# Kernel tuning notes

Hardware: AMD Instinct MI355X
Metric: run time of the kernel (lower is better)

The kernel has to match this reference:

```python
import jax, jax.numpy as jnp
import numpy as np

B, T, D, K = 32, 2048, 1024, 31


def setup_inputs() -> dict:
    key = jax.random.key(0)
    ks = jax.random.split(key, 8)
    query = jax.random.normal(ks[0], (B, D), dtype=jnp.float32)
    memory = jax.random.normal(ks[1], (B, T, D), dtype=jnp.float32)
    prev_attn = jax.nn.softmax(jax.random.normal(ks[2], (B, T)), axis=-1).astype(jnp.float32)
    cum_attn = jax.random.uniform(ks[3], (B, T), dtype=jnp.float32)
    mask = jax.random.bernoulli(ks[4], 0.2, (B, T))
    mask = mask.at[:, 0].set(False)  # keep at least one valid position per row
    scale = 0.02
    Wq = jax.random.normal(ks[5], (D, D), dtype=jnp.float32) * scale    # torch Linear weight [out,in]
    Wm = jax.random.normal(ks[6], (D, D), dtype=jnp.float32) * scale
    k2 = jax.random.split(ks[7], 2)
    Wloc = jax.random.normal(k2[0], (D, 2, K), dtype=jnp.float32) * scale  # Conv1d weight [out_ch,in_ch,k]
    v = jax.random.normal(k2[1], (D,), dtype=jnp.float32) * scale          # Linear(d_model,1) weight squeezed
    return {"query": query, "memory": memory, "prev_attn": prev_attn,
            "cum_attn": cum_attn, "mask": mask,
            "Wq": Wq, "Wm": Wm, "Wloc": Wloc, "v": v}


def reference(query, memory, prev_attn, cum_attn, mask, Wq, Wm, Wloc, v):
    pad = Wloc.shape[-1] // 2
    # location features: [B,2,T] conv -> [B,D,T] -> [B,T,D]
    loc_in = jnp.stack([prev_attn, cum_attn], axis=1)
    loc = jax.lax.conv_general_dilated(
        loc_in, Wloc, window_strides=(1,), padding=[(pad, pad)],
        dimension_numbers=("NCW", "OIW", "NCW"))
    loc = jnp.transpose(loc, (0, 2, 1))                 # [B,T,D]
    q = (query @ Wq.T)[:, None, :]                      # [B,1,D]
    m = jnp.einsum("btd,ed->bte", memory, Wm)           # [B,T,D]
    e = jnp.einsum("btd,d->bt", jnp.tanh(q + m + loc), v)  # [B,T]
    e = jnp.where(mask, -jnp.inf, e)
    a = jax.nn.softmax(e, axis=1)                       # [B,T]
    ctx = jnp.einsum("bt,btd->bd", a, memory)           # [B,D]
    return ctx, a
```

## Files before the change

kernel.cpp:

```cpp
#include <hip/hip_runtime.h>
#include <math.h>

#define BATCH 32
#define T 2048
#define D 1024
#define KW 31
#define CPAD 15
#define KEXT 62
#define KEXTP 64
#define KTOT 1088
#define BM 128
#define BN 128
#define BK 32
#define NSTEP (KTOT / BK)

typedef __bf16 bf16_8 __attribute__((ext_vector_type(8)));
typedef __bf16 bf16_4 __attribute__((ext_vector_type(4)));
typedef float  f32x4  __attribute__((ext_vector_type(4)));

__device__ __forceinline__ float tanh_fast(float x) {
    return 1.f - 2.f * __builtin_amdgcn_rcpf(__expf(2.f * x) + 1.f);
}

__device__ __forceinline__ void glds16(const void* gsrc, void* ldst) {
    __builtin_amdgcn_global_load_lds(
        (const __attribute__((address_space(1))) unsigned int*)gsrc,
        (__attribute__((address_space(3))) unsigned int*)ldst, 16, 0, 0);
}

__global__ __launch_bounds__(256) void k_prep_b(const float* __restrict__ Wm,
                                                const float* __restrict__ Wloc,
                                                __bf16* __restrict__ Bext) {
    const int idx = blockIdx.x * 256 + threadIdx.x;
    const int d = idx / (KTOT / 4);
    const int kk = (idx % (KTOT / 4)) * 4;
    bf16_4 o;
    #pragma unroll
    for (int u = 0; u < 4; ++u) {
        const int k = kk + u;
        float val = 0.f;
        if (k < D) val = Wm[(size_t)d * D + k];
        else {
            const int j = k - D;
            if (j < KEXT) {
                const int c = (j >= KW) ? 1 : 0;
                const int kp = j - c * KW;
                val = Wloc[((size_t)d * 2 + c) * KW + kp];
            }
        }
        o[u] = (__bf16)val;
    }
    *(bf16_4*)(Bext + (size_t)d * KTOT + kk) = o;
}

__global__ __launch_bounds__(256) void k_prep_aloc(const float* __restrict__ prev,
                                                   const float* __restrict__ cum,
                                                   __bf16* __restrict__ Aloc) {
    const int idx = blockIdx.x * 256 + threadIdx.x;
    const int row = idx >> 4;
    const int j0 = (idx & 15) * 4;
    const int b = row >> 11;
    const int t = row & (T - 1);
    bf16_4 o;
    #pragma unroll
    for (int u = 0; u < 4; ++u) {
        const int j = j0 + u;
        float val = 0.f;
        if (j < KEXT) {
            const int c = (j >= KW) ? 1 : 0;
            const int kp = j - c * KW;
            const int ts = t + kp - CPAD;
            if (ts >= 0 && ts < T)
                val = (c ? cum : prev)[(size_t)b * T + ts];
        }
        o[u] = (__bf16)val;
    }
    *(bf16_4*)(Aloc + (size_t)row * KEXTP + j0) = o;
}

__global__ __launch_bounds__(256) void k_q(const float* __restrict__ query,
                                           const float* __restrict__ Wq,
                                           float* __restrict__ qout) {
    int b = blockIdx.y;
    int w = threadIdx.x >> 6;
    int lane = threadIdx.x & 63;
    int d = blockIdx.x * 4 + w;
    const float* qrow = query + (size_t)b * D;
    const float* wrow = Wq + (size_t)d * D;
    float s = 0.f;
    #pragma unroll
    for (int i = 0; i < D / 64; ++i) s += qrow[lane + i * 64] * wrow[lane + i * 64];
    #pragma unroll
    for (int off = 32; off > 0; off >>= 1) s += __shfl_down(s, off, 64);
    if (lane == 0) qout[(size_t)b * D + d] = s;
}

__global__ __launch_bounds__(256, 3) void k_gemm_e(
    const float* __restrict__ memory, const __bf16* __restrict__ Aloc,
    const __bf16* __restrict__ Bext, const float* __restrict__ qv,
    const float* __restrict__ vvec, float* __restrict__ e_part) {
    __shared__ bf16_8 As[3][512];
    __shared__ bf16_8 Bs[3][512];

    const int t0 = blockIdx.x * BM;
    const int d0 = blockIdx.y * BN;
    const int b  = blockIdx.z;
    const int tid  = threadIdx.x;
    const int lane = tid & 63;
    const int w    = tid >> 6;
    const int wr   = w >> 1, wc = w & 1;
    const int q    = lane >> 4, m = lane & 15;

    f32x4 acc[4][4] = {};

    const int g0 = w, g1 = w + 4;
    const size_t arow0 = (size_t)b * T + t0 + g0 * 16 + m;
    const size_t arow1 = (size_t)b * T + t0 + g1 * 16 + m;
    const float*  aptr0 = memory + arow0 * D + q * 8;
    const float*  aptr1 = memory + arow1 * D + q * 8;
    const __bf16* lptr0 = Aloc + arow0 * KEXTP + q * 8;
    const __bf16* lptr1 = Aloc + arow1 * KEXTP + q * 8;
    const __bf16* bptr0 = Bext + (size_t)(d0 + g0 * 16 + m) * KTOT + q * 8;
    const __bf16* bptr1 = Bext + (size_t)(d0 + g1 * 16 + m) * KTOT + q * 8;

    f32x4 pa[2][2];

    glds16(bptr0,      &Bs[0][g0 * 64]);
    glds16(bptr1,      &Bs[0][g1 * 64]);
    glds16(bptr0 + BK, &Bs[1][g0 * 64]);
    glds16(bptr1 + BK, &Bs[1][g1 * 64]);
    pa[0][0] = *(const f32x4*)(aptr0);
    pa[0][1] = *(const f32x4*)(aptr0 + 4);
    pa[1][0] = *(const f32x4*)(aptr1);
    pa[1][1] = *(const f32x4*)(aptr1 + 4);
    {
        bf16_8 c0, c1;
        #pragma unroll
        for (int i = 0; i < 4; ++i) {
            c0[i] = (__bf16)pa[0][0][i]; c0[i + 4] = (__bf16)pa[0][1][i];
            c1[i] = (__bf16)pa[1][0][i]; c1[i + 4] = (__bf16)pa[1][1][i];
        }
        As[0][g0 * 64 + lane] = c0;
        As[0][g1 * 64 + lane] = c1;
    }

    for (int k = 0; k < NSTEP; ++k) {
        const int p = k % 3;
        if (k > 0 && k * BK < D) {
            bf16_8 c0, c1;
            #pragma unroll
            for (int i = 0; i < 4; ++i) {
                c0[i] = (__bf16)pa[0][0][i]; c0[i + 4] = (__bf16)pa[0][1][i];
                c1[i] = (__bf16)pa[1][0][i]; c1[i + 4] = (__bf16)pa[1][1][i];
            }
            As[p][g0 * 64 + lane] = c0;
            As[p][g1 * 64 + lane] = c1;
        }
        __syncthreads();
        const int ka = k + 1;
        if (ka < NSTEP) {
            const int ka0 = ka * BK;
            if (ka0 < D) {
                pa[0][0] = *(const f32x4*)(aptr0 + ka0);
                pa[0][1] = *(const f32x4*)(aptr0 + ka0 + 4);
                pa[1][0] = *(const f32x4*)(aptr1 + ka0);
                pa[1][1] = *(const f32x4*)(aptr1 + ka0 + 4);
            } else {
                glds16(lptr0 + (ka0 - D), &As[ka % 3][g0 * 64]);
                glds16(lptr1 + (ka0 - D), &As[ka % 3][g1 * 64]);
            }
        }
        const int kb = k + 2;
        if (kb < NSTEP) {
            glds16(bptr0 + kb * BK, &Bs[kb % 3][g0 * 64]);
            glds16(bptr1 + kb * BK, &Bs[kb % 3][g1 * 64]);
        }
        bf16_8 af[4], bfr[4];
        #pragma unroll
        for (int i = 0; i < 4; ++i) af[i]  = As[p][(wr * 4 + i) * 64 + lane];
        #pragma unroll
        for (int j = 0; j < 4; ++j) bfr[j] = Bs[p][(wc * 4 + j) * 64 + lane];
        #pragma unroll
        for (int i = 0; i < 4; ++i)
            #pragma unroll
            for (int j = 0; j < 4; ++j)
                acc[i][j] = __builtin_amdgcn_mfma_f32_16x16x32_bf16(af[i], bfr[j], acc[i][j], 0, 0, 0);
    }

    float qreg[4], vreg[4];
    #pragma unroll
    for (int j = 0; j < 4; ++j) {
        const int d = d0 + wc * 64 + j * 16 + m;
        qreg[j] = qv[(size_t)b * D + d];
        vreg[j] = vvec[d];
    }
    const int dch = blockIdx.y * 2 + wc;
    #pragma unroll
    for (int i = 0; i < 4; ++i) {
        #pragma unroll
        for (int r = 0; r < 4; ++r) {
            float s = 0.f;
            #pragma unroll
            for (int j = 0; j < 4; ++j)
                s += tanh_fast(acc[i][j][r] + qreg[j]) * vreg[j];
            #pragma unroll
            for (int off = 8; off > 0; off >>= 1)
                s += __shfl_down(s, off, 16);
            if (m == 0) {
                const int t = t0 + wr * 64 + i * 16 + q * 4 + r;
                e_part[((size_t)b * T + t) * 16 + dch] = s;
            }
        }
    }
}

__global__ __launch_bounds__(256) void k_softmax(const float* __restrict__ e_part,
                                                 const int* __restrict__ mask,
                                                 float* __restrict__ aout) {
    const int b = blockIdx.x;
    const int tid = threadIdx.x;
    __shared__ float red[256];
    float ev[8];
    float lmax = -INFINITY;
    #pragma unroll
    for (int i = 0; i < 8; ++i) {
        const int t = tid + i * 256;
        const float* p = e_part + ((size_t)b * T + t) * 16;
        float s = 0.f;
        #pragma unroll
        for (int c = 0; c < 16; ++c) s += p[c];
        if (mask[(size_t)b * T + t] != 0) s = -INFINITY;
        ev[i] = s;
        lmax = fmaxf(lmax, s);
    }
    red[tid] = lmax; __syncthreads();
    for (int off = 128; off > 0; off >>= 1) {
        if (tid < off) red[tid] = fmaxf(red[tid], red[tid + off]);
        __syncthreads();
    }
    const float mx = red[0]; __syncthreads();
    float lsum = 0.f;
    #pragma unroll
    for (int i = 0; i < 8; ++i) {
        const float x = expf(ev[i] - mx);
        ev[i] = x;
        lsum += x;
    }
    red[tid] = lsum; __syncthreads();
    for (int off = 128; off > 0; off >>= 1) {
        if (tid < off) red[tid] += red[tid + off];
        __syncthreads();
    }
    const float inv = 1.f / red[0];
    #pragma unroll
    for (int i = 0; i < 8; ++i)
        aout[(size_t)b * T + tid + i * 256] = ev[i] * inv;
}

__global__ __launch_bounds__(256) void k_ctx_part(const float* __restrict__ memory,
                                                  const float* __restrict__ a,
                                                  float* __restrict__ ctx_part) {
    const int b = blockIdx.x;
    const int tc = blockIdx.y;
    const int d4 = threadIdx.x * 4;
    f32x4 acc = {0.f, 0.f, 0.f, 0.f};
    const float* mb = memory + ((size_t)b * T + (size_t)tc * 64) * D;
    const float* ab = a + (size_t)b * T + (size_t)tc * 64;
    #pragma unroll 4
    for (int t = 0; t < 64; ++t) {
        const float wgt = ab[t];
        const f32x4 m4 = *(const f32x4*)(mb + (size_t)t * D + d4);
        acc += wgt * m4;
    }
    *(f32x4*)(ctx_part + ((size_t)(b * 32 + tc)) * D + d4) = acc;
}

__global__ __launch_bounds__(256) void k_ctx_red(const float* __restrict__ ctx_part,
                                                 float* __restrict__ ctx) {
    const int idx = blockIdx.x * 256 + threadIdx.x;
    const int b = idx >> 10, d = idx & 1023;
    float s = 0.f;
    #pragma unroll
    for (int tc = 0; tc < 32; ++tc) s += ctx_part[((size_t)(b * 32 + tc)) * D + d];
    ctx[idx] = s;
}

extern "C" void kernel_launch(void* const* d_in, const int* in_sizes, int n_in,
                              void* d_out, int out_size, void* d_ws, size_t ws_size,
                              hipStream_t stream) {
    const float* query  = (const float*)d_in[0];
    const float* memory = (const float*)d_in[1];
    const float* prev   = (const float*)d_in[2];
    const float* cum    = (const float*)d_in[3];
    const int*   mask   = (const int*)d_in[4];
    const float* Wq     = (const float*)d_in[5];
    const float* Wm     = (const float*)d_in[6];
    const float* Wloc   = (const float*)d_in[7];
    const float* v      = (const float*)d_in[8];

    float* out = (float*)d_out;
    float* ctx = out;
    float* a   = out + BATCH * D;

    char* ws = (char*)d_ws;
    float*  qv       = (float*)(ws + 0);
    float*  e_part   = (float*)(ws + 131072);
    float*  ctx_part = (float*)(ws + 4325376);
    __bf16* Bext     = (__bf16*)(ws + 8519680);
    __bf16* Aloc     = (__bf16*)(ws + 10747904);

    k_prep_b<<<KTOT * D / (256 * 4), 256, 0, stream>>>(Wm, Wloc, Bext);
    k_prep_aloc<<<BATCH * T * 16 / 256, 256, 0, stream>>>(prev, cum, Aloc);
    k_q<<<dim3(D / 4, BATCH), 256, 0, stream>>>(query, Wq, qv);
    k_gemm_e<<<dim3(T / BM, D / BN, BATCH), 256, 0, stream>>>(memory, Aloc, Bext,
                                                              qv, v, e_part);
    k_softmax<<<BATCH, 256, 0, stream>>>(e_part, mask, a);
    k_ctx_part<<<dim3(BATCH, 32), 256, 0, stream>>>(memory, a, ctx_part);
    k_ctx_red<<<(BATCH * D) / 256, 256, 0, stream>>>(ctx_part, ctx);
}
```

Measured before the change: 759.7 us.

## Drop LDS staging in GEMM, load fragments directly from global, reorder grid

The energy GEMM no longer stages tiles in LDS with a triple-buffered async pipeline and barriers. Each wave now loads its A (fp32 memory, converted to bf16) and B fragments straight from global memory into registers, and the location-feature K tail becomes a separate loop. The grid is reordered so the D tiles of the same T rows run adjacently, which should improve L2 reuse of memory rows, and occupancy is raised to 4 blocks per CU. Without LDS sharing, each memory element is fetched by both column waves and B is fetched per row wave, which doubles global/L2 traffic. The softmax kernel also moves to 1024 threads with vectorised partial-sum loads.

Measured after the change: 1.073 ms. 41.2% more time.

```diff
diff --git a/kernel.cpp b/kernel.cpp
--- a/kernel.cpp
+++ b/kernel.cpp
@@ -12,7 +12,6 @@
 #define BM 128
 #define BN 128
 #define BK 32
-#define NSTEP (KTOT / BK)
 
 typedef __bf16 bf16_8 __attribute__((ext_vector_type(8)));
 typedef __bf16 bf16_4 __attribute__((ext_vector_type(4)));
@@ -20,12 +19,6 @@
 
 __device__ __forceinline__ float tanh_fast(float x) {
     return 1.f - 2.f * __builtin_amdgcn_rcpf(__expf(2.f * x) + 1.f);
-}
-
-__device__ __forceinline__ void glds16(const void* gsrc, void* ldst) {
-    __builtin_amdgcn_global_load_lds(
-        (const __attribute__((address_space(1))) unsigned int*)gsrc,
-        (__attribute__((address_space(3))) unsigned int*)ldst, 16, 0, 0);
 }
 
 __global__ __launch_bounds__(256) void k_prep_b(const float* __restrict__ Wm,
@@ -95,15 +88,12 @@
     if (lane == 0) qout[(size_t)b * D + d] = s;
 }
 
-__global__ __launch_bounds__(256, 3) void k_gemm_e(
+__global__ __launch_bounds__(256, 4) void k_gemm_e(
     const float* __restrict__ memory, const __bf16* __restrict__ Aloc,
     const __bf16* __restrict__ Bext, const float* __restrict__ qv,
     const float* __restrict__ vvec, float* __restrict__ e_part) {
-    __shared__ bf16_8 As[3][512];
-    __shared__ bf16_8 Bs[3][512];
-
-    const int t0 = blockIdx.x * BM;
-    const int d0 = blockIdx.y * BN;
+    const int d0 = blockIdx.x * BN;
+    const int t0 = blockIdx.y * BM;
     const int b  = blockIdx.z;
     const int tid  = threadIdx.x;
     const int lane = tid & 63;
@@ -113,73 +103,47 @@
 
     f32x4 acc[4][4] = {};
 
-    const int g0 = w, g1 = w + 4;
-    const size_t arow0 = (size_t)b * T + t0 + g0 * 16 + m;
-    const size_t arow1 = (size_t)b * T + t0 + g1 * 16 + m;
-    const float*  aptr0 = memory + arow0 * D + q * 8;
-    const float*  aptr1 = memory + arow1 * D + q * 8;
-    const __bf16* lptr0 = Aloc + arow0 * KEXTP + q * 8;
-    const __bf16* lptr1 = Aloc + arow1 * KEXTP + q * 8;
-    const __bf16* bptr0 = Bext + (size_t)(d0 + g0 * 16 + m) * KTOT + q * 8;
-    const __bf16* bptr1 = Bext + (size_t)(d0 + g1 * 16 + m) * KTOT + q * 8;
-
-    f32x4 pa[2][2];
-
-    glds16(bptr0,      &Bs[0][g0 * 64]);
-    glds16(bptr1,      &Bs[0][g1 * 64]);
-    glds16(bptr0 + BK, &Bs[1][g0 * 64]);
-    glds16(bptr1 + BK, &Bs[1][g1 * 64]);
-    pa[0][0] = *(const f32x4*)(aptr0);
-    pa[0][1] = *(const f32x4*)(aptr0 + 4);
-    pa[1][0] = *(const f32x4*)(aptr1);
-    pa[1][1] = *(const f32x4*)(aptr1 + 4);
-    {
-        bf16_8 c0, c1;
+    const float*  mb = memory + (size_t)b * T * D;
+    int aoff[4], boff[4];
+    #pragma unroll
+    for (int i = 0; i < 4; ++i)
+        aoff[i] = (t0 + wr * 64 + i * 16 + m) * D + q * 8;
+    #pragma unroll
+    for (int j = 0; j < 4; ++j)
+        boff[j] = (d0 + wc * 64 + j * 16 + m) * KTOT + q * 8;
+
+    #pragma unroll 2
+    for (int k0 = 0; k0 < D; k0 += BK) {
+        bf16_8 af[4], bfr[4];
         #pragma unroll
         for (int i = 0; i < 4; ++i) {
-            c0[i] = (__bf16)pa[0][0][i]; c0[i + 4] = (__bf16)pa[0][1][i];
-            c1[i] = (__bf16)pa[1][0][i]; c1[i + 4] = (__bf16)pa[1][1][i];
-        }
-        As[0][g0 * 64 + lane] = c0;
-        As[0][g1 * 64 + lane] = c1;
-    }
-
-    for (int k = 0; k < NSTEP; ++k) {
-        const int p = k % 3;
-        if (k > 0 && k * BK < D) {
-            bf16_8 c0, c1;
-            #pragma unroll
-            for (int i = 0; i < 4; ++i) {
-                c0[i] = (__bf16)pa[0][0][i]; c0[i + 4] = (__bf16)pa[0][1][i];
-                c1[i] = (__bf16)pa[1][0][i]; c1[i + 4] = (__bf16)pa[1][1][i];
+            const f32x4 x = *(const f32x4*)(mb + aoff[i] + k0);
+            const f32x4 y = *(const f32x4*)(mb + aoff[i] + k0 + 4);
+            #pragma unroll
+            for (int u = 0; u < 4; ++u) {
+                af[i][u]     = (__bf16)x[u];
+                af[i][u + 4] = (__bf16)y[u];
             }
-            As[p][g0 * 64 + lane] = c0;
-            As[p][g1 * 64 + lane] = c1;
-        }
-        __syncthreads();
-        const int ka = k + 1;
-        if (ka < NSTEP) {
-            const int ka0 = ka * BK;
-            if (ka0 < D) {
-                pa[0][0] = *(const f32x4*)(aptr0 + ka0);
-                pa[0][1] = *(const f32x4*)(aptr0 + ka0 + 4);
-                pa[1][0] = *(const f32x4*)(aptr1 + ka0);
-                pa[1][1] = *(const f32x4*)(aptr1 + ka0 + 4);
-            } else {
-                glds16(lptr0 + (ka0 - D), &As[ka % 3][g0 * 64]);
-                glds16(lptr1 + (ka0 - D), &As[ka % 3][g1 * 64]);
-            }
-        }
-        const int kb = k + 2;
-        if (kb < NSTEP) {
-            glds16(bptr0 + kb * BK, &Bs[kb % 3][g0 * 64]);
-            glds16(bptr1 + kb * BK, &Bs[kb % 3][g1 * 64]);
-        }
+        }
+        #pragma unroll
+        for (int j = 0; j < 4; ++j)
+            bfr[j] = *(const bf16_8*)(Bext + boff[j] + k0);
+        #pragma unroll
+        for (int i = 0; i < 4; ++i)
+            #pragma unroll
+            for (int j = 0; j < 4; ++j)
+                acc[i][j] = __builtin_amdgcn_mfma_f32_16x16x32_bf16(af[i], bfr[j], acc[i][j], 0, 0, 0);
+    }
+    const __bf16* lb = Aloc + (size_t)b * T * KEXTP;
+    #pragma unroll
+    for (int k0 = 0; k0 < KEXTP; k0 += BK) {
         bf16_8 af[4], bfr[4];
         #pragma unroll
-        for (int i = 0; i < 4; ++i) af[i]  = As[p][(wr * 4 + i) * 64 + lane];
-        #pragma unroll
-        for (int j = 0; j < 4; ++j) bfr[j] = Bs[p][(wc * 4 + j) * 64 + lane];
+        for (int i = 0; i < 4; ++i)
+            af[i] = *(const bf16_8*)(lb + (t0 + wr * 64 + i * 16 + m) * KEXTP + q * 8 + k0);
+        #pragma unroll
+        for (int j = 0; j < 4; ++j)
+            bfr[j] = *(const bf16_8*)(Bext + boff[j] + D + k0);
         #pragma unroll
         for (int i = 0; i < 4; ++i)
             #pragma unroll
@@ -194,7 +158,7 @@
         qreg[j] = qv[(size_t)b * D + d];
         vreg[j] = vvec[d];
     }
-    const int dch = blockIdx.y * 2 + wc;
+    const int dch = blockIdx.x * 2 + wc;
     #pragma unroll
     for (int i = 0; i < 4; ++i) {
         #pragma unroll
@@ -214,47 +178,48 @@
     }
 }
 
-__global__ __launch_bounds__(256) void k_softmax(const float* __restrict__ e_part,
-                                                 const int* __restrict__ mask,
-                                                 float* __restrict__ aout) {
+__global__ __launch_bounds__(1024) void k_softmax(const float* __restrict__ e_part,
+                                                  const int* __restrict__ mask,
+                                                  float* __restrict__ aout) {
     const int b = blockIdx.x;
     const int tid = threadIdx.x;
-    __shared__ float red[256];
-    float ev[8];
+    __shared__ float red[1024];
+    float ev[2];
     float lmax = -INFINITY;
     #pragma unroll
-    for (int i = 0; i < 8; ++i) {
-        const int t = tid + i * 256;
+    for (int i = 0; i < 2; ++i) {
+        const int t = tid + i * 1024;
         const float* p = e_part + ((size_t)b * T + t) * 16;
-        float s = 0.f;
-        #pragma unroll
-        for (int c = 0; c < 16; ++c) s += p[c];
+        f32x4 s4 = {0.f, 0.f, 0.f, 0.f};
+        #pragma unroll
+        for (int c = 0; c < 4; ++c) s4 += *(const f32x4*)(p + c * 4);
+        float s = s4[0] + s4[1] + s4[2] + s4[3];
         if (mask[(size_t)b * T + t] != 0) s = -INFINITY;
         ev[i] = s;
         lmax = fmaxf(lmax, s);
     }
     red[tid] = lmax; __syncthreads();
-    for (int off = 128; off > 0; off >>= 1) {
+    for (int off = 512; off > 0; off >>= 1) {
         if (tid < off) red[tid] = fmaxf(red[tid], red[tid + off]);
         __syncthreads();
     }
     const float mx = red[0]; __syncthreads();
     float lsum = 0.f;
     #pragma unroll
-    for (int i = 0; i < 8; ++i) {
+    for (int i = 0; i < 2; ++i) {
         const float x = expf(ev[i] - mx);
         ev[i] = x;
         lsum += x;
     }
     red[tid] = lsum; __syncthreads();
-    for (int off = 128; off > 0; off >>= 1) {
+    for (int off = 512; off > 0; off >>= 1) {
         if (tid < off) red[tid] += red[tid + off];
         __syncthreads();
     }
     const float inv = 1.f / red[0];
     #pragma unroll
-    for (int i = 0; i < 8; ++i)
-        aout[(size_t)b * T + tid + i * 256] = ev[i] * inv;
+    for (int i = 0; i < 2; ++i)
+        aout[(size_t)b * T + tid + i * 1024] = ev[i] * inv;
 }
 
 __global__ __launch_bounds__(256) void k_ctx_part(const float* __restrict__ memory,
@@ -312,9 +277,9 @@
     k_prep_b<<<KTOT * D / (256 * 4), 256, 0, stream>>>(Wm, Wloc, Bext);
     k_prep_aloc<<<BATCH * T * 16 / 256, 256, 0, stream>>>(prev, cum, Aloc);
     k_q<<<dim3(D / 4, BATCH), 256, 0, stream>>>(query, Wq, qv);
-    k_gemm_e<<<dim3(T / BM, D / BN, BATCH), 256, 0, stream>>>(memory, Aloc, Bext,
+    k_gemm_e<<<dim3(D / BN, T / BM, BATCH), 256, 0, stream>>>(memory, Aloc, Bext,
                                                               qv, v, e_part);
-    k_softmax<<<BATCH, 256, 0, stream>>>(e_part, mask, a);
+    k_softmax<<<BATCH, 1024, 0, stream>>>(e_part, mask, a);
     k_ctx_part<<<dim3(BATCH, 32), 256, 0, stream>>>(memory, a, ctx_part);
     k_ctx_red<<<(BATCH * D) / 256, 256, 0, stream>>>(ctx_part, ctx);
 }
```
